# Kernel tuning notes

Measured on AMD Instinct MI355X. Metric: run time of the kernel, lower is better.

Reference implementation:

```python
import jax, jax.numpy as jnp
import numpy as np

B, S, QD, KVD, H = 8, 1024, 1024, 1024, 8
NEG_SLOPE = 0.01


def _lin(t, w, b):
    # torch nn.Linear: y = x @ W^T + b, W is (out, in)
    return t @ w.T + b


def _heads(t, n_head):
    b, s, e = t.shape
    return t.reshape(b, s, n_head, e // n_head).transpose(0, 2, 1, 3)  # (B,H,S,D)


def _merge(t):
    b, h, s, d = t.shape
    return t.transpose(0, 2, 1, 3).reshape(b, s, h * d)


def setup_inputs() -> dict:
    key = jax.random.key(0)
    ks = iter(jax.random.split(key, 64))

    def W(shape):
        return (jax.random.normal(next(ks), shape, jnp.float32) * 0.02)

    inp = {
        'x': jax.random.normal(next(ks), (B, S, QD), jnp.float32),
        'y': jax.random.normal(next(ks), (B, S, KVD), jnp.float32),
        # cross-attention projections
        'ca_q_w': W((QD, QD)), 'ca_q_b': W((QD,)),
        'ca_qv_w': W((QD, QD)), 'ca_qv_b': W((QD,)),
        'ca_k_w': W((QD, KVD)), 'ca_k_b': W((QD,)),
        'ca_kv_w': W((QD, KVD)), 'ca_kv_b': W((QD,)),
        'ca_o_w': W((QD, QD)), 'ca_o_b': W((QD,)),
        # LayerNorm over [seq_len, q_dim]
        'ln_w': jnp.ones((S, QD), jnp.float32),
        'ln_b': jnp.zeros((S, QD), jnp.float32),
        # 3-layer FeedForward
        'ff1_w': W((QD, QD)), 'ff1_b': W((QD,)),
        'ff2_w': W((QD, QD)), 'ff2_b': W((QD,)),
        'ff3_w': W((QD, QD)), 'ff3_b': W((QD,)),
        # self-attention 1
        'sa1_q_w': W((QD, QD)), 'sa1_q_b': W((QD,)),
        'sa1_k_w': W((QD, QD)), 'sa1_k_b': W((QD,)),
        'sa1_v_w': W((QD, QD)), 'sa1_v_b': W((QD,)),
        'sa1_o_w': W((QD, QD)), 'sa1_o_b': W((QD,)),
        # self-attention 2
        'sa2_q_w': W((QD, QD)), 'sa2_q_b': W((QD,)),
        'sa2_k_w': W((QD, QD)), 'sa2_k_b': W((QD,)),
        'sa2_v_w': W((QD, QD)), 'sa2_v_b': W((QD,)),
        'sa2_o_w': W((QD, QD)), 'sa2_o_b': W((QD,)),
    }
    return inp


def _self_attn(t, qw, qb, kw, kb, vw, vb, ow, ob):
    q = _heads(_lin(t, qw, qb), H)
    k = _heads(_lin(t, kw, kb), H)
    v = _heads(_lin(t, vw, vb), H)
    scale = 1.0 / jnp.sqrt(jnp.asarray(q.shape[-1], q.dtype))
    a = jax.nn.softmax(jnp.einsum('bhsd,bhtd->bhst', q, k) * scale, axis=-1)
    return _lin(_merge(jnp.einsum('bhst,bhtd->bhsd', a, v)), ow, ob)


def reference(x, y, ca_q_w, ca_q_b, ca_qv_w, ca_qv_b, ca_k_w, ca_k_b, ca_kv_w, ca_kv_b, ca_o_w, ca_o_b, ln_w, ln_b, ff1_w, ff1_b, ff2_w, ff2_b, ff3_w, ff3_b, sa1_q_w, sa1_q_b, sa1_k_w, sa1_k_b, sa1_v_w, sa1_v_b, sa1_o_w, sa1_o_b, sa2_q_w, sa2_q_b, sa2_k_w, sa2_k_b, sa2_v_w, sa2_v_b, sa2_o_w, sa2_o_b):
    # --- FlowFace cross-attention (no 1/sqrt(d) scaling, +QV term) ---
    q = _heads(_lin(x, ca_q_w, ca_q_b), H)
    qv = _heads(_lin(x, ca_qv_w, ca_qv_b), H)
    k = _heads(_lin(y, ca_k_w, ca_k_b), H)
    kv = _heads(_lin(y, ca_kv_w, ca_kv_b), H)
    attn = jax.nn.softmax(jnp.einsum('bhsd,bhtd->bhst', q, k), axis=-1)
    ca = _lin(_merge(jnp.einsum('bhst,bhtd->bhsd', attn, kv) + qv), ca_o_w, ca_o_b)
    h1 = x + ca
    # --- LayerNorm over last two dims [seq_len, q_dim] ---
    mu = h1.mean(axis=(-2, -1), keepdims=True)
    var = h1.var(axis=(-2, -1), keepdims=True)
    hn = (h1 - mu) / jnp.sqrt(var + 1e-5) * ln_w + ln_b
    # --- 3-layer FeedForward with leaky_relu + residual ---
    lr = lambda t: jax.nn.leaky_relu(t, NEG_SLOPE)
    f = lr(_lin(lr(_lin(lr(_lin(hn, ff1_w, ff1_b)), ff2_w, ff2_b)), ff3_w, ff3_b))
    h2 = hn + f
    # --- two self-attention layers ---
    h3 = _self_attn(h2, sa1_q_w, sa1_q_b, sa1_k_w, sa1_k_b, sa1_v_w, sa1_v_b, sa1_o_w, sa1_o_b)
    out = _self_attn(h3, sa2_q_w, sa2_q_b, sa2_k_w, sa2_k_b, sa2_v_w, sa2_v_b, sa2_o_w, sa2_o_b)
    return out
```

## Files before the change

kernel.cpp:

```cpp
#include <hip/hip_runtime.h>
#include <cstdint>
#include <cstddef>

#define DI __device__ __forceinline__

typedef __bf16 bf16x8 __attribute__((ext_vector_type(8)));
typedef float  f32x4  __attribute__((ext_vector_type(4)));

constexpr int kE = 1024;
constexpr int kM = 8192;
constexpr float kSlope = 0.01f;

DI float bf2f(ushort u) { union { uint32_t i; float f; } v; v.i = ((uint32_t)u) << 16; return v.f; }
DI ushort f2bf(float f) {
    union { float f; uint32_t i; } v; v.f = f;
    return (ushort)((v.i + 0x7FFFu + ((v.i >> 16) & 1u)) >> 16);
}
DI bf16x8 ld8f(const float* p) {
    const float4 f0 = *(const float4*)p;
    const float4 f1 = *(const float4*)(p + 4);
    union { bf16x8 v; ushort u[8]; } o;
    o.u[0] = f2bf(f0.x); o.u[1] = f2bf(f0.y); o.u[2] = f2bf(f0.z); o.u[3] = f2bf(f0.w);
    o.u[4] = f2bf(f1.x); o.u[5] = f2bf(f1.y); o.u[6] = f2bf(f1.z); o.u[7] = f2bf(f1.w);
    return o.v;
}
template<typename T> DI float ldf(const T* p);
template<> DI float ldf<ushort>(const ushort* p) { return bf2f(*p); }
template<> DI float ldf<float>(const float* p) { return *p; }

DI void gload16(const void* g, void* lds) {
    __builtin_amdgcn_global_load_lds((const __attribute__((address_space(1))) void*)g,
                                     (__attribute__((address_space(3))) void*)lds, 16, 0, 0);
}

DI int swz7(int r) { return ((r ^ (r >> 3)) & 7) << 4; }

struct PtrTab { const float* w[16]; const float* b[16]; const float* x; const float* y; };

__global__ __launch_bounds__(256)
void cvt_pack(PtrTab t, ushort* __restrict__ WB, ushort* __restrict__ Xb,
              ushort* __restrict__ Yb, float* __restrict__ BP)
{
    const int blk = blockIdx.x, tid = threadIdx.x;
    if (blk < 16384) {
        const float* src; ushort* dst; size_t idx;
        if (blk < 8192)       { const int w = blk >> 9; idx = (size_t)(blk & 511) * 2048 + tid * 8; src = t.w[w]; dst = WB + (size_t)w * 1048576; }
        else if (blk < 12288) { idx = (size_t)(blk - 8192) * 2048 + tid * 8;  src = t.x; dst = Xb; }
        else                  { idx = (size_t)(blk - 12288) * 2048 + tid * 8; src = t.y; dst = Yb; }
        *(bf16x8*)(dst + idx) = ld8f(src + idx);
    } else {
        const size_t i = (size_t)(blk - 16384) * 2048 + tid * 8;
        const int w = (int)(i >> 10), off = (int)(i & 1023);
        *(float4*)(BP + i)     = *(const float4*)(t.b[w] + off);
        *(float4*)(BP + i + 4) = *(const float4*)(t.b[w] + off + 4);
    }
}

template<int ACT, int RESID, int VT, typename TR, typename TO>
__global__ __launch_bounds__(256)
void gemm_bf16(const ushort* __restrict__ A, const ushort* __restrict__ W,
               const float* __restrict__ bias, const TR* __restrict__ resb,
               TO* __restrict__ out, int N, ushort* __restrict__ vt_out, int vtcol0)
{
    __shared__ __align__(16) char sm[2][16384];
    constexpr int K = 1024;
    const int tid = threadIdx.x, l = tid & 63, wid = tid >> 6;
    const int wm = wid >> 1, wn = wid & 1;

    const int cpx = gridDim.x >> 3;
    const int sb = (blockIdx.x & 7) * cpx + (blockIdx.x >> 3);
    const int slab = sb >> 9, rr = sb & 511;
    const int bm = rr >> 3, bn = (slab << 3) + (rr & 7);
    const size_t row0 = (size_t)bm << 7, col0 = (size_t)bn << 7;
    const bool isvt = VT && ((int)col0 >= vtcol0);

    const int o0 = (wid * 2) * 1024 + (l << 4), o1 = o0 + 1024;
    const int r0s = o0 >> 6, c0s = ((o0 >> 4) & 3) ^ ((r0s >> 1) & 3);
    const int r1s = o1 >> 6, c1s = ((o1 >> 4) & 3) ^ ((r1s >> 1) & 3);
    const ushort* gA0 = A + (row0 + r0s) * K + c0s * 8;
    const ushort* gA1 = A + (row0 + r1s) * K + c1s * 8;
    const ushort* gW0 = W + (col0 + r0s) * K + c0s * 8;
    const ushort* gW1 = W + (col0 + r1s) * K + c1s * 8;
    const int d0 = (wid * 2) * 1024, d1 = d0 + 1024;

    f32x4 acc[4][4] = {};

    {
        gload16(gA0, sm[0] + d0); gload16(gA1, sm[0] + d1);
        gload16(gW0, sm[0] + 8192 + d0); gload16(gW1, sm[0] + 8192 + d1);
    }
    __syncthreads();

    for (int kt = 0; kt < 32; ++kt) {
        const int cur = kt & 1;
        if (kt + 1 < 32) {
            const int ko = (kt + 1) << 5;
            char* nb = sm[cur ^ 1];
            gload16(gA0 + ko, nb + d0); gload16(gA1 + ko, nb + d1);
            gload16(gW0 + ko, nb + 8192 + d0); gload16(gW1 + ko, nb + 8192 + d1);
        }
        const char* At = sm[cur];
        const char* Wt = sm[cur] + 8192;
        bf16x8 af[4], bfr[4];
        #pragma unroll
        for (int mi = 0; mi < 4; ++mi) {
            const int r = (wm << 6) + (mi << 4) + (l & 15);
            af[mi] = *(const bf16x8*)(At + r * 64 + ((((l >> 4) ^ ((r >> 1) & 3))) << 4));
        }
        #pragma unroll
        for (int ni = 0; ni < 4; ++ni) {
            const int r = (wn << 6) + (ni << 4) + (l & 15);
            bfr[ni] = *(const bf16x8*)(Wt + r * 64 + ((((l >> 4) ^ ((r >> 1) & 3))) << 4));
        }
        if (!isvt) {
            #pragma unroll
            for (int mi = 0; mi < 4; ++mi)
                #pragma unroll
                for (int ni = 0; ni < 4; ++ni)
                    acc[mi][ni] = __builtin_amdgcn_mfma_f32_16x16x32_bf16(af[mi], bfr[ni], acc[mi][ni], 0, 0, 0);
        } else {
            #pragma unroll
            for (int mi = 0; mi < 4; ++mi)
                #pragma unroll
                for (int ni = 0; ni < 4; ++ni)
                    acc[mi][ni] = __builtin_amdgcn_mfma_f32_16x16x32_bf16(bfr[ni], af[mi], acc[mi][ni], 0, 0, 0);
        }
        __syncthreads();
    }

    const int cr = (l >> 4) << 2, cc = l & 15;
    if (!isvt) {
        #pragma unroll
        for (int mi = 0; mi < 4; ++mi) {
            #pragma unroll
            for (int ni = 0; ni < 4; ++ni) {
                const size_t gr = row0 + (wm << 6) + (mi << 4) + cr;
                const size_t gc = col0 + (wn << 6) + (ni << 4) + cc;
                const float bv = bias[gc];
                #pragma unroll
                for (int r = 0; r < 4; ++r) {
                    float v = acc[mi][ni][r] + bv;
                    if (ACT) v = v > 0.f ? v : v * kSlope;
                    const size_t off = (gr + r) * (size_t)N + gc;
                    if (RESID) v += ldf(resb + off);
                    if constexpr (sizeof(TO) == 4) out[off] = v;
                    else                           out[off] = f2bf(v);
                }
            }
        }
    } else if (VT) {
        #pragma unroll
        for (int mi = 0; mi < 4; ++mi) {
            const size_t t_glob = row0 + (wm << 6) + (mi << 4) + cc;
            const size_t bb = t_glob >> 10;
            const int tt = (int)(t_glob & 1023);
            #pragma unroll
            for (int ni = 0; ni < 4; ++ni) {
                const int gcb = (int)col0 + (wn << 6) + (ni << 4) + cr;
                const int dbase = gcb - vtcol0;
                #pragma unroll
                for (int r = 0; r < 4; ++r) {
                    const float v = acc[mi][ni][r] + bias[gcb + r];
                    vt_out[(((bb << 10) + dbase + r) << 10) + tt] = f2bf(v);
                }
            }
        }
    }
}

template<int ADD_QV>
__global__ __launch_bounds__(256)
void attn_fwd(const ushort* __restrict__ Q, const ushort* __restrict__ K,
              const ushort* __restrict__ VT, const ushort* __restrict__ QV,
              ushort* __restrict__ O, int ld, float scale)
{
    __shared__ __align__(16) char Kt[64 * 256];
    __shared__ __align__(16) char Vt[128 * 128];
    __shared__ __align__(16) char Pl[4][2048];

    const int tid = threadIdx.x;
    const int l = tid & 63, w = tid >> 6;

    const int cpx = gridDim.x >> 3;
    const int sb = (blockIdx.x & 7) * cpx + (blockIdx.x >> 3);
    const int qt = sb & 15;
    const int bh = sb >> 4;
    const int h = bh & 7, b = bh >> 3;

    const size_t bi = ((size_t)b << 10) * (size_t)ld + ((size_t)h << 7);
    const size_t bo = ((size_t)b << 10) * 1024 + ((size_t)h << 7);
    const size_t vtoff = ((size_t)bh) << 17;
    const size_t qrow0 = (size_t)(qt << 6) + (w << 4);

    bf16x8 qf[4];
    #pragma unroll
    for (int kk = 0; kk < 4; ++kk)
        qf[kk] = *(const bf16x8*)(Q + bi + (qrow0 + (l & 15)) * ld + (kk << 5) + ((l >> 4) << 3));

    f32x4 oacc[8] = {};
    f32x4 lacc = {};
    float mrow[4] = {-1e30f, -1e30f, -1e30f, -1e30f};

    bf16x8 vones;
    #pragma unroll
    for (int j = 0; j < 8; ++j) vones[j] = (__bf16)1.0f;

    const int sr = tid >> 4, sc = tid & 15;

    int vofs[4];
    #pragma unroll
    for (int it = 0; it < 4; ++it) {
        const int d = it * 32 + (tid >> 3);
        const int s = tid & 7;
        const int c = s ^ ((d ^ (d >> 3)) & 7);
        vofs[it] = d * 1024 + c * 8;
    }
    const int vdst = tid * 16;

    for (int kt0 = 0; kt0 < 16; ++kt0) {
        __syncthreads();
        #pragma unroll
        for (int it = 0; it < 4; ++it) {
            const int r = sr + (it << 4);
            uint4 kv = *(const uint4*)(K + bi + (size_t)(kt0 * 64 + r) * ld + (sc << 3));
            *(uint4*)(Kt + r * 256 + ((sc << 4) ^ swz7(r))) = kv;
        }
        #pragma unroll
        for (int it = 0; it < 4; ++it) {
            uint4 vv = *(const uint4*)(VT + vtoff + (size_t)(kt0 << 6) + vofs[it]);
            *(uint4*)(Vt + it * 4096 + vdst) = vv;
        }
        __syncthreads();

        f32x4 sacc[4] = {};
        #pragma unroll
        for (int ni = 0; ni < 4; ++ni) {
            const int r = (l & 15) + (ni << 4);
            #pragma unroll
            for (int kk = 0; kk < 4; ++kk) {
                bf16x8 kf = *(const bf16x8*)(Kt + r * 256 + ((((kk << 2) + (l >> 4)) << 4) ^ swz7(r)));
                sacc[ni] = __builtin_amdgcn_mfma_f32_16x16x32_bf16(qf[kk], kf, sacc[ni], 0, 0, 0);
            }
        }
        #pragma unroll
        for (int ni = 0; ni < 4; ++ni) sacc[ni] *= scale;

        float m0[4];
        #pragma unroll
        for (int r = 0; r < 4; ++r) {
            float m = fmaxf(fmaxf(sacc[0][r], sacc[1][r]), fmaxf(sacc[2][r], sacc[3][r]));
            #pragma unroll
            for (int msk = 1; msk < 16; msk <<= 1) m = fmaxf(m, __shfl_xor(m, msk, 64));
            m0[r] = m;
        }
        const bool grow = (m0[0] > mrow[0]) || (m0[1] > mrow[1]) ||
                          (m0[2] > mrow[2]) || (m0[3] > mrow[3]);
        if (__any(grow)) {
            float corr[4];
            #pragma unroll
            for (int r = 0; r < 4; ++r) {
                const float mn = fmaxf(mrow[r], m0[r]);
                corr[r] = __expf(mrow[r] - mn);
                mrow[r] = mn;
            }
            #pragma unroll
            for (int nd = 0; nd < 8; ++nd)
                #pragma unroll
                for (int r = 0; r < 4; ++r) oacc[nd][r] *= corr[r];
            #pragma unroll
            for (int r = 0; r < 4; ++r) lacc[r] *= corr[r];
        }

        char* pw = Pl[w];
        #pragma unroll
        for (int r = 0; r < 4; ++r) {
            const int q = ((l >> 4) << 2) + r;
            const int qo = q * 128, qm = swz7(q);
            const float mr = mrow[r];
            #pragma unroll
            for (int ni = 0; ni < 4; ++ni) {
                const float p = __expf(sacc[ni][r] - mr);
                const int t = (l & 15) + (ni << 4);
                *(__bf16*)(pw + qo + ((t * 2) ^ qm)) = (__bf16)p;
            }
        }

        #pragma unroll
        for (int tg = 0; tg < 2; ++tg) {
            const int q = l & 15;
            bf16x8 pf = *(const bf16x8*)(pw + q * 128 + ((((tg << 2) + (l >> 4)) << 4) ^ swz7(q)));
            #pragma unroll
            for (int nd = 0; nd < 8; ++nd) {
                const int d = (nd << 4) + (l & 15);
                const int m = (d ^ (d >> 3)) & 7;
                bf16x8 vf = *(const bf16x8*)(Vt + d * 128 + ((((tg << 2) + (l >> 4)) ^ m) << 4));
                oacc[nd] = __builtin_amdgcn_mfma_f32_16x16x32_bf16(pf, vf, oacc[nd], 0, 0, 0);
            }
            lacc = __builtin_amdgcn_mfma_f32_16x16x32_bf16(pf, vones, lacc, 0, 0, 0);
        }
    }

    const size_t orow = qrow0 + ((l >> 4) << 2);
    #pragma unroll
    for (int r = 0; r < 4; ++r) {
        const float inv = 1.f / lacc[r];
        #pragma unroll
        for (int nd = 0; nd < 8; ++nd) {
            const size_t c = (l & 15) + (nd << 4);
            float v = oacc[nd][r] * inv;
            if (ADD_QV) v += bf2f(QV[bi + (orow + r) * ld + c]);
            O[bo + (orow + r) * 1024 + c] = f2bf(v);
        }
    }
}

__global__ void ln_partial(const ushort* __restrict__ h1, float2* __restrict__ part)
{
    __shared__ float sa[8];
    const size_t off = ((size_t)blockIdx.x) << 15;
    float s = 0.f, s2 = 0.f;
    for (int i = threadIdx.x; i < 4096; i += 256) {
        uint4 u = *(const uint4*)(h1 + off + (size_t)i * 8);
        const ushort* e = (const ushort*)&u;
        #pragma unroll
        for (int j = 0; j < 8; ++j) { const float v = bf2f(e[j]); s += v; s2 += v * v; }
    }
    #pragma unroll
    for (int m = 1; m < 64; m <<= 1) { s += __shfl_xor(s, m, 64); s2 += __shfl_xor(s2, m, 64); }
    const int w = threadIdx.x >> 6;
    if ((threadIdx.x & 63) == 0) { sa[w * 2] = s; sa[w * 2 + 1] = s2; }
    __syncthreads();
    if (threadIdx.x == 0)
        part[blockIdx.x] = make_float2(sa[0] + sa[2] + sa[4] + sa[6], sa[1] + sa[3] + sa[5] + sa[7]);
}

__global__ void ln_finish(const float2* __restrict__ part, float2* __restrict__ stats)
{
    const int b = threadIdx.x;
    if (b < 8) {
        float s = 0.f, s2 = 0.f;
        for (int c = 0; c < 32; ++c) { const float2 v = part[b * 32 + c]; s += v.x; s2 += v.y; }
        const float mu = s * (1.f / 1048576.f);
        const float var = s2 * (1.f / 1048576.f) - mu * mu;
        stats[b] = make_float2(mu, rsqrtf(var + 1e-5f));
    }
}

__global__ void ln_apply(const ushort* __restrict__ h1, const float2* __restrict__ stats,
                         const float* __restrict__ gw, const float* __restrict__ gb,
                         ushort* __restrict__ hn)
{
    const size_t i = ((size_t)blockIdx.x * 256 + threadIdx.x) * 8;
    const int b = (int)(i >> 20);
    const size_t r = i & 1048575;
    const float2 st = stats[b];
    uint4 uv = *(const uint4*)(h1 + i);
    const float4 w0 = *(const float4*)(gw + r);
    const float4 w1 = *(const float4*)(gw + r + 4);
    const float4 b0 = *(const float4*)(gb + r);
    const float4 b1 = *(const float4*)(gb + r + 4);
    const float wv[8] = {w0.x, w0.y, w0.z, w0.w, w1.x, w1.y, w1.z, w1.w};
    const float bv[8] = {b0.x, b0.y, b0.z, b0.w, b1.x, b1.y, b1.z, b1.w};
    const ushort* ev = (const ushort*)&uv;
    ushort o[8];
    #pragma unroll
    for (int j = 0; j < 8; ++j)
        o[j] = f2bf((bf2f(ev[j]) - st.x) * st.y * wv[j] + bv[j]);
    *(uint4*)(hn + i) = *(const uint4*)o;
}

extern "C" void kernel_launch(void* const* d_in, const int* in_sizes, int n_in,
                              void* d_out, int out_size, void* d_ws, size_t ws_size,
                              hipStream_t stream)
{
    (void)in_sizes; (void)n_in; (void)out_size; (void)ws_size;
    auto P = [&](int i) { return (const float*)d_in[i]; };

    const size_t MB = 1u << 20;
    char* ws = (char*)d_ws;
    ushort* WB = (ushort*)ws;
    ushort* B0 = (ushort*)(ws + 32 * MB);
    ushort* B1 = (ushort*)(ws + 48 * MB);
    ushort* B2 = (ushort*)(ws + 64 * MB);
    ushort* B3 = (ushort*)(ws + 80 * MB);
    ushort* B4 = (ushort*)(ws + 96 * MB);
    ushort* B5 = (ushort*)(ws + 112 * MB);
    float*  BP = (float*)(ws + 128 * MB);
    float2* PART = (float2*)(ws + 128 * MB + 65536);
    float2* STATS = PART + 256;

    PtrTab tab;
    const int wsrc[16] = {2,4,6,8,10,14,16,18,20,22,24,26,28,30,32,34};
    for (int i = 0; i < 16; ++i) { tab.w[i] = P(wsrc[i]); tab.b[i] = P(wsrc[i] + 1); }
    tab.x = P(0); tab.y = P(1);

    const dim3 blk(256), gg(512);
    const float SA_SCALE = 0.08838834764831845f;
    auto Wp = [&](int w) { return WB + (size_t)w * 1048576; };
    auto Bp = [&](int w) { return BP + (size_t)w * 1024; };
    const ushort* NUS = nullptr;

    cvt_pack<<<dim3(16392), blk, 0, stream>>>(tab, WB, B4, B5, BP);

    gemm_bf16<0,0,0,ushort,ushort><<<gg, blk, 0, stream>>>(B4, Wp(0), Bp(0), NUS, B0, 1024, nullptr, 0);
    gemm_bf16<0,0,0,ushort,ushort><<<gg, blk, 0, stream>>>(B4, Wp(1), Bp(1), NUS, B1, 1024, nullptr, 0);
    gemm_bf16<0,0,0,ushort,ushort><<<gg, blk, 0, stream>>>(B5, Wp(2), Bp(2), NUS, B2, 1024, nullptr, 0);
    gemm_bf16<0,0,1,ushort,ushort><<<gg, blk, 0, stream>>>(B5, Wp(3), Bp(3), NUS, B3, 1024, B3, 0);
    attn_fwd<1><<<dim3(1024), blk, 0, stream>>>(B0, B2, B3, B1, B4, 1024, 1.0f);
    gemm_bf16<0,1,0,float,ushort><<<gg, blk, 0, stream>>>(B4, Wp(4), Bp(4), P(0), B5, 1024, nullptr, 0);

    ln_partial<<<dim3(256), blk, 0, stream>>>(B5, PART);
    ln_finish<<<dim3(1), dim3(64), 0, stream>>>(PART, STATS);
    ln_apply<<<dim3(4096), blk, 0, stream>>>(B5, STATS, P(12), P(13), B0);

    gemm_bf16<1,0,0,ushort,ushort><<<gg, blk, 0, stream>>>(B0, Wp(5), Bp(5), NUS, B1, 1024, nullptr, 0);
    gemm_bf16<1,0,0,ushort,ushort><<<gg, blk, 0, stream>>>(B1, Wp(6), Bp(6), NUS, B2, 1024, nullptr, 0);
    gemm_bf16<1,1,0,ushort,ushort><<<gg, blk, 0, stream>>>(B2, Wp(7), Bp(7), B0, B3, 1024, nullptr, 0);

    gemm_bf16<0,0,0,ushort,ushort><<<gg, blk, 0, stream>>>(B3, Wp(8),  Bp(8),  NUS, B0, 1024, nullptr, 0);
    gemm_bf16<0,0,0,ushort,ushort><<<gg, blk, 0, stream>>>(B3, Wp(9),  Bp(9),  NUS, B1, 1024, nullptr, 0);
    gemm_bf16<0,0,1,ushort,ushort><<<gg, blk, 0, stream>>>(B3, Wp(10), Bp(10), NUS, B2, 1024, B2, 0);
    attn_fwd<0><<<dim3(1024), blk, 0, stream>>>(B0, B1, B2, nullptr, B4, 1024, SA_SCALE);
    gemm_bf16<0,0,0,ushort,ushort><<<gg, blk, 0, stream>>>(B4, Wp(11), Bp(11), NUS, B5, 1024, nullptr, 0);

    gemm_bf16<0,0,0,ushort,ushort><<<gg, blk, 0, stream>>>(B5, Wp(12), Bp(12), NUS, B0, 1024, nullptr, 0);
    gemm_bf16<0,0,0,ushort,ushort><<<gg, blk, 0, stream>>>(B5, Wp(13), Bp(13), NUS, B1, 1024, nullptr, 0);
    gemm_bf16<0,0,1,ushort,ushort><<<gg, blk, 0, stream>>>(B5, Wp(14), Bp(14), NUS, B2, 1024, B2, 0);
    attn_fwd<0><<<dim3(1024), blk, 0, stream>>>(B0, B1, B2, nullptr, B4, 1024, SA_SCALE);
    gemm_bf16<0,0,0,ushort,float><<<gg, blk, 0, stream>>>(B4, Wp(15), Bp(15), NUS, (float*)d_out, 1024, nullptr, 0);
}
```

Measured before the change: 757.2 us.

## Transpose attention MFMA layout and fold softmax scale into Q projection

The attention kernel swaps MFMA operand order so each lane holds one query row's scores. Row max then needs only two cross-lane shuffles, and the rescale and max tracking become scalar per lane. Output stores become 4-wide vector writes. The 1/sqrt(d) scale is moved into the Q-projection GEMM epilogue, so the per-tile score multiply disappears, but Q is now rounded to bf16 after scaling.

```diff
diff --git a/kernel.cpp b/kernel.cpp
--- a/kernel.cpp
+++ b/kernel.cpp
@@ -60,7 +60,8 @@
 __global__ __launch_bounds__(256)
 void gemm_bf16(const ushort* __restrict__ A, const ushort* __restrict__ W,
                const float* __restrict__ bias, const TR* __restrict__ resb,
-               TO* __restrict__ out, int N, ushort* __restrict__ vt_out, int vtcol0)
+               TO* __restrict__ out, int N, ushort* __restrict__ vt_out, int vtcol0,
+               float oscale)
 {
     __shared__ __align__(16) char sm[2][16384];
     constexpr int K = 1024;
@@ -139,7 +140,7 @@
                 const float bv = bias[gc];
                 #pragma unroll
                 for (int r = 0; r < 4; ++r) {
-                    float v = acc[mi][ni][r] + bv;
+                    float v = (acc[mi][ni][r] + bv) * oscale;
                     if (ACT) v = v > 0.f ? v : v * kSlope;
                     const size_t off = (gr + r) * (size_t)N + gc;
                     if (RESID) v += ldf(resb + off);
@@ -172,7 +173,7 @@
 __global__ __launch_bounds__(256)
 void attn_fwd(const ushort* __restrict__ Q, const ushort* __restrict__ K,
               const ushort* __restrict__ VT, const ushort* __restrict__ QV,
-              ushort* __restrict__ O, int ld, float scale)
+              ushort* __restrict__ O, int ld)
 {
     __shared__ __align__(16) char Kt[64 * 256];
     __shared__ __align__(16) char Vt[128 * 128];
@@ -185,10 +186,10 @@
     const int sb = (blockIdx.x & 7) * cpx + (blockIdx.x >> 3);
     const int qt = sb & 15;
     const int bh = sb >> 4;
-    const int h = bh & 7, b = bh >> 3;
-
-    const size_t bi = ((size_t)b << 10) * (size_t)ld + ((size_t)h << 7);
-    const size_t bo = ((size_t)b << 10) * 1024 + ((size_t)h << 7);
+    const int h8 = bh & 7, b = bh >> 3;
+
+    const size_t bi = ((size_t)b << 10) * (size_t)ld + ((size_t)h8 << 7);
+    const size_t bo = ((size_t)b << 10) * 1024 + ((size_t)h8 << 7);
     const size_t vtoff = ((size_t)bh) << 17;
     const size_t qrow0 = (size_t)(qt << 6) + (w << 4);
 
@@ -199,7 +200,7 @@
 
     f32x4 oacc[8] = {};
     f32x4 lacc = {};
-    float mrow[4] = {-1e30f, -1e30f, -1e30f, -1e30f};
+    float mrow = -1e30f;
 
     bf16x8 vones;
     #pragma unroll
@@ -217,6 +218,9 @@
     }
     const int vdst = tid * 16;
 
+    const int q = l & 15, hh = l >> 4;
+    const int qo = q * 128, qm = swz7(q);
+
     for (int kt0 = 0; kt0 < 16; ++kt0) {
         __syncthreads();
         #pragma unroll
@@ -239,78 +243,67 @@
             #pragma unroll
             for (int kk = 0; kk < 4; ++kk) {
                 bf16x8 kf = *(const bf16x8*)(Kt + r * 256 + ((((kk << 2) + (l >> 4)) << 4) ^ swz7(r)));
-                sacc[ni] = __builtin_amdgcn_mfma_f32_16x16x32_bf16(qf[kk], kf, sacc[ni], 0, 0, 0);
+                sacc[ni] = __builtin_amdgcn_mfma_f32_16x16x32_bf16(kf, qf[kk], sacc[ni], 0, 0, 0);
             }
         }
-        #pragma unroll
-        for (int ni = 0; ni < 4; ++ni) sacc[ni] *= scale;
-
-        float m0[4];
-        #pragma unroll
-        for (int r = 0; r < 4; ++r) {
-            float m = fmaxf(fmaxf(sacc[0][r], sacc[1][r]), fmaxf(sacc[2][r], sacc[3][r]));
-            #pragma unroll
-            for (int msk = 1; msk < 16; msk <<= 1) m = fmaxf(m, __shfl_xor(m, msk, 64));
-            m0[r] = m;
-        }
-        const bool grow = (m0[0] > mrow[0]) || (m0[1] > mrow[1]) ||
-                          (m0[2] > mrow[2]) || (m0[3] > mrow[3]);
-        if (__any(grow)) {
-            float corr[4];
+
+        float m0 = sacc[0][0];
+        #pragma unroll
+        for (int ni = 0; ni < 4; ++ni)
+            #pragma unroll
+            for (int r = 0; r < 4; ++r) m0 = fmaxf(m0, sacc[ni][r]);
+        m0 = fmaxf(m0, __shfl_xor(m0, 16, 64));
+        m0 = fmaxf(m0, __shfl_xor(m0, 32, 64));
+
+        if (__any(m0 > mrow)) {
+            const float mn = fmaxf(mrow, m0);
+            const float corr = __expf(mrow - mn);
+            mrow = mn;
+            #pragma unroll
+            for (int nd = 0; nd < 8; ++nd) oacc[nd] *= corr;
+            lacc *= corr;
+        }
+
+        char* pw = Pl[w];
+        #pragma unroll
+        for (int ni = 0; ni < 4; ++ni)
             #pragma unroll
             for (int r = 0; r < 4; ++r) {
-                const float mn = fmaxf(mrow[r], m0[r]);
-                corr[r] = __expf(mrow[r] - mn);
-                mrow[r] = mn;
-            }
-            #pragma unroll
-            for (int nd = 0; nd < 8; ++nd)
-                #pragma unroll
-                for (int r = 0; r < 4; ++r) oacc[nd][r] *= corr[r];
-            #pragma unroll
-            for (int r = 0; r < 4; ++r) lacc[r] *= corr[r];
-        }
-
-        char* pw = Pl[w];
-        #pragma unroll
-        for (int r = 0; r < 4; ++r) {
-            const int q = ((l >> 4) << 2) + r;
-            const int qo = q * 128, qm = swz7(q);
-            const float mr = mrow[r];
-            #pragma unroll
-            for (int ni = 0; ni < 4; ++ni) {
-                const float p = __expf(sacc[ni][r] - mr);
-                const int t = (l & 15) + (ni << 4);
+                const float p = __expf(sacc[ni][r] - mrow);
+                const int t = (ni << 4) + (hh << 2) + r;
                 *(__bf16*)(pw + qo + ((t * 2) ^ qm)) = (__bf16)p;
             }
-        }
 
         #pragma unroll
         for (int tg = 0; tg < 2; ++tg) {
-            const int q = l & 15;
-            bf16x8 pf = *(const bf16x8*)(pw + q * 128 + ((((tg << 2) + (l >> 4)) << 4) ^ swz7(q)));
+            bf16x8 pf = *(const bf16x8*)(pw + qo + ((((tg << 2) + hh) << 4) ^ qm));
+            lacc = __builtin_amdgcn_mfma_f32_16x16x32_bf16(vones, pf, lacc, 0, 0, 0);
             #pragma unroll
             for (int nd = 0; nd < 8; ++nd) {
                 const int d = (nd << 4) + (l & 15);
                 const int m = (d ^ (d >> 3)) & 7;
                 bf16x8 vf = *(const bf16x8*)(Vt + d * 128 + ((((tg << 2) + (l >> 4)) ^ m) << 4));
-                oacc[nd] = __builtin_amdgcn_mfma_f32_16x16x32_bf16(pf, vf, oacc[nd], 0, 0, 0);
+                oacc[nd] = __builtin_amdgcn_mfma_f32_16x16x32_bf16(vf, pf, oacc[nd], 0, 0, 0);
             }
-            lacc = __builtin_amdgcn_mfma_f32_16x16x32_bf16(pf, vones, lacc, 0, 0, 0);
-        }
-    }
-
-    const size_t orow = qrow0 + ((l >> 4) << 2);
-    #pragma unroll
-    for (int r = 0; r < 4; ++r) {
-        const float inv = 1.f / lacc[r];
-        #pragma unroll
-        for (int nd = 0; nd < 8; ++nd) {
-            const size_t c = (l & 15) + (nd << 4);
-            float v = oacc[nd][r] * inv;
-            if (ADD_QV) v += bf2f(QV[bi + (orow + r) * ld + c]);
-            O[bo + (orow + r) * 1024 + c] = f2bf(v);
-        }
+        }
+    }
+
+    const size_t row = qrow0 + q;
+    const float inv = 1.f / lacc[0];
+    #pragma unroll
+    for (int nd = 0; nd < 8; ++nd) {
+        const int dd0 = (nd << 4) + (hh << 2);
+        ushort o4[4];
+        if (ADD_QV) {
+            uint2 qv4 = *(const uint2*)(QV + bi + row * ld + dd0);
+            const ushort* qe = (const ushort*)&qv4;
+            #pragma unroll
+            for (int r = 0; r < 4; ++r) o4[r] = f2bf(oacc[nd][r] * inv + bf2f(qe[r]));
+        } else {
+            #pragma unroll
+            for (int r = 0; r < 4; ++r) o4[r] = f2bf(oacc[nd][r] * inv);
+        }
+        *(uint2*)(O + bo + row * 1024 + dd0) = *(const uint2*)o4;
     }
 }
 
@@ -402,30 +395,30 @@
 
     cvt_pack<<<dim3(16392), blk, 0, stream>>>(tab, WB, B4, B5, BP);
 
-    gemm_bf16<0,0,0,ushort,ushort><<<gg, blk, 0, stream>>>(B4, Wp(0), Bp(0), NUS, B0, 1024, nullptr, 0);
-    gemm_bf16<0,0,0,ushort,ushort><<<gg, blk, 0, stream>>>(B4, Wp(1), Bp(1), NUS, B1, 1024, nullptr, 0);
-    gemm_bf16<0,0,0,ushort,ushort><<<gg, blk, 0, stream>>>(B5, Wp(2), Bp(2), NUS, B2, 1024, nullptr, 0);
-    gemm_bf16<0,0,1,ushort,ushort><<<gg, blk, 0, stream>>>(B5, Wp(3), Bp(3), NUS, B3, 1024, B3, 0);
-    attn_fwd<1><<<dim3(1024), blk, 0, stream>>>(B0, B2, B3, B1, B4, 1024, 1.0f);
-    gemm_bf16<0,1,0,float,ushort><<<gg, blk, 0, stream>>>(B4, Wp(4), Bp(4), P(0), B5, 1024, nullptr, 0);
+    gemm_bf16<0,0,0,ushort,ushort><<<gg, blk, 0, stream>>>(B4, Wp(0), Bp(0), NUS, B0, 1024, nullptr, 0, 1.0f);
+    gemm_bf16<0,0,0,ushort,ushort><<<gg, blk, 0, stream>>>(B4, Wp(1), Bp(1), NUS, B1, 1024, nullptr, 0, 1.0f);
+    gemm_bf16<0,0,0,ushort,ushort><<<gg, blk, 0, stream>>>(B5, Wp(2), Bp(2), NUS, B2, 1024, nullptr, 0, 1.0f);
+    gemm_bf16<0,0,1,ushort,ushort><<<gg, blk, 0, stream>>>(B5, Wp(3), Bp(3), NUS, B3, 1024, B3, 0, 1.0f);
+    attn_fwd<1><<<dim3(1024), blk, 0, stream>>>(B0, B2, B3, B1, B4, 1024);
+    gemm_bf16<0,1,0,float,ushort><<<gg, blk, 0, stream>>>(B4, Wp(4), Bp(4), P(0), B5, 1024, nullptr, 0, 1.0f);
 
     ln_partial<<<dim3(256), blk, 0, stream>>>(B5, PART);
     ln_finish<<<dim3(1), dim3(64), 0, stream>>>(PART, STATS);
     ln_apply<<<dim3(4096), blk, 0, stream>>>(B5, STATS, P(12), P(13), B0);
 
-    gemm_bf16<1,0,0,ushort,ushort><<<gg, blk, 0, stream>>>(B0, Wp(5), Bp(5), NUS, B1, 1024, nullptr, 0);
-    gemm_bf16<1,0,0,ushort,ushort><<<gg, blk, 0, stream>>>(B1, Wp(6), Bp(6), NUS, B2, 1024, nullptr, 0);
-    gemm_bf16<1,1,0,ushort,ushort><<<gg, blk, 0, stream>>>(B2, Wp(7), Bp(7), B0, B3, 1024, nullptr, 0);
-
-    gemm_bf16<0,0,0,ushort,ushort><<<gg, blk, 0, stream>>>(B3, Wp(8),  Bp(8),  NUS, B0, 1024, nullptr, 0);
-    gemm_bf16<0,0,0,ushort,ushort><<<gg, blk, 0, stream>>>(B3, Wp(9),  Bp(9),  NUS, B1, 1024, nullptr, 0);
-    gemm_bf16<0,0,1,ushort,ushort><<<gg, blk, 0, stream>>>(B3, Wp(10), Bp(10), NUS, B2, 1024, B2, 0);
-    attn_fwd<0><<<dim3(1024), blk, 0, stream>>>(B0, B1, B2, nullptr, B4, 1024, SA_SCALE);
-    gemm_bf16<0,0,0,ushort,ushort><<<gg, blk, 0, stream>>>(B4, Wp(11), Bp(11), NUS, B5, 1024, nullptr, 0);
-
-    gemm_bf16<0,0,0,ushort,ushort><<<gg, blk, 0, stream>>>(B5, Wp(12), Bp(12), NUS, B0, 1024, nullptr, 0);
-    gemm_bf16<0,0,0,ushort,ushort><<<gg, blk, 0, stream>>>(B5, Wp(13), Bp(13), NUS, B1, 1024, nullptr, 0);
-    gemm_bf16<0,0,1,ushort,ushort><<<gg, blk, 0, stream>>>(B5, Wp(14), Bp(14), NUS, B2, 1024, B2, 0);
-    attn_fwd<0><<<dim3(1024), blk, 0, stream>>>(B0, B1, B2, nullptr, B4, 1024, SA_SCALE);
-    gemm_bf16<0,0,0,ushort,float><<<gg, blk, 0, stream>>>(B4, Wp(15), Bp(15), NUS, (float*)d_out, 1024, nullptr, 0);
-}
+    gemm_bf16<1,0,0,ushort,ushort><<<gg, blk, 0, stream>>>(B0, Wp(5), Bp(5), NUS, B1, 1024, nullptr, 0, 1.0f);
+    gemm_bf16<1,0,0,ushort,ushort><<<gg, blk, 0, stream>>>(B1, Wp(6), Bp(6), NUS, B2, 1024, nullptr, 0, 1.0f);
+    gemm_bf16<1,1,0,ushort,ushort><<<gg, blk, 0, stream>>>(B2, Wp(7), Bp(7), B0, B3, 1024, nullptr, 0, 1.0f);
+
+    gemm_bf16<0,0,0,ushort,ushort><<<gg, blk, 0, stream>>>(B3, Wp(8),  Bp(8),  NUS, B0, 1024, nullptr, 0, SA_SCALE);
+    gemm_bf16<0,0,0,ushort,ushort><<<gg, blk, 0, stream>>>(B3, Wp(9),  Bp(9),  NUS, B1, 1024, nullptr, 0, 1.0f);
+    gemm_bf16<0,0,1,ushort,ushort><<<gg, blk, 0, stream>>>(B3, Wp(10), Bp(10), NUS, B2, 1024, B2, 0, 1.0f);
+    attn_fwd<0><<<dim3(1024), blk, 0, stream>>>(B0, B1, B2, nullptr, B4, 1024);
+    gemm_bf16<0,0,0,ushort,ushort><<<gg, blk, 0, stream>>>(B4, Wp(11), Bp(11), NUS, B5, 1024, nullptr, 0, 1.0f);
+
+    gemm_bf16<0,0,0,ushort,ushort><<<gg, blk, 0, stream>>>(B5, Wp(12), Bp(12), NUS, B0, 1024, nullptr, 0, SA_SCALE);
+    gemm_bf16<0,0,0,ushort,ushort><<<gg, blk, 0, stream>>>(B5, Wp(13), Bp(13), NUS, B1, 1024, nullptr, 0, 1.0f);
+    gemm_bf16<0,0,1,ushort,ushort><<<gg, blk, 0, stream>>>(B5, Wp(14), Bp(14), NUS, B2, 1024, B2, 0, 1.0f);
+    attn_fwd<0><<<dim3(1024), blk, 0, stream>>>(B0, B1, B2, nullptr, B4, 1024);
+    gemm_bf16<0,0,0,ushort,float><<<gg, blk, 0, stream>>>(B4, Wp(15), Bp(15), NUS, (float*)d_out, 1024, nullptr, 0, 1.0f);
+}
```

Result: slower. 894.9 us (+18.2%).
